# Kernel optimization log

Hardware: AMD Instinct MI355X
Metric: run time of the kernel (lower is better)

## Reference

```python
import jax, jax.numpy as jnp
import numpy as np

LMBDA = 0.95
RHO_MAX = 1.0
C_MAX = 1.0
N, T = 8192, 1024


def setup_inputs() -> dict:
    key = jax.random.key(0)
    ks = jax.random.split(key, 7)
    gammas = jax.random.uniform(ks[0], (N, T), dtype=jnp.float32) * 0.02 + 0.97  # discounts near 0.99
    vf_x = jax.random.normal(ks[1], (N, T + 1), dtype=jnp.float32)
    rewards = jax.random.normal(ks[2], (N, T), dtype=jnp.float32)
    action_lls = jax.random.normal(ks[3], (N, T), dtype=jnp.float32) * 0.1
    original_action_lls = jax.random.normal(ks[4], (N, T), dtype=jnp.float32) * 0.1
    terminated = jax.random.randint(ks[5], (N,), 0, 2) > 0
    episode_lengths = jax.random.randint(ks[6], (N,), 1, T + 1)
    return {
        "gammas": gammas,
        "vf_x": vf_x,
        "rewards": rewards,
        "action_lls": action_lls,
        "original_action_lls": original_action_lls,
        "terminated": terminated,
        "episode_lengths": episode_lengths,
    }


def reference(gammas, vf_x, rewards, action_lls, original_action_lls, terminated, episode_lengths):
    n_episodes, max_len = rewards.shape
    importance_weight = jnp.exp(action_lls - original_action_lls)
    rho = jnp.minimum(importance_weight, RHO_MAX)
    ep_idx = jnp.arange(n_episodes)
    # zero out discount at final step of terminated episodes
    gammas = gammas.at[ep_idx, episode_lengths - 1].multiply((~terminated).astype(gammas.dtype))
    c = LMBDA * jnp.minimum(importance_weight, C_MAX)
    gamma_c = gammas * c  # (N, T)
    delta_V = rho * (rewards + gammas * vf_x[:, 1:] - vf_x[:, :-1])  # (N, T)

    # backward recurrence: v_diff[t] = delta_V[t] + gamma_c[t] * v_diff[t+1], v_diff[T] = 0
    def step(carry, inp):
        dV_t, gc_t = inp  # each (N,)
        v = dV_t + gc_t * carry
        return v, v

    init = jnp.zeros((n_episodes,), dtype=vf_x.dtype)
    _, ys = jax.lax.scan(step, init, (delta_V.T[::-1], gamma_c.T[::-1]))  # ys: (T, N) reversed time
    v_diff = jnp.concatenate([ys[::-1].T, jnp.zeros((n_episodes, 1), dtype=vf_x.dtype)], axis=1)  # (N, T+1)
    v_s = v_diff + vf_x
    advantages = rho * (rewards * gammas * v_s[:, 1:] - vf_x[:, :-1])
    return advantages, v_s
```

## Files before the change

kernel.cpp:

```cpp
#include <hip/hip_runtime.h>

static constexpr int N_EP  = 8192;
static constexpr int T_LEN = 1024;
static constexpr float LMBDA = 0.95f;

__global__ __launch_bounds__(256) void vtrace_kernel(
    const float* __restrict__ gammas,
    const float* __restrict__ vf_x,
    const float* __restrict__ rewards,
    const float* __restrict__ action_lls,
    const float* __restrict__ orig_lls,
    const int*   __restrict__ terminated,
    const int*   __restrict__ ep_len,
    float* __restrict__ adv_out,
    float* __restrict__ vs_out)
{
    const int n    = blockIdx.x * 4 + (threadIdx.x >> 6);
    const int lane = threadIdx.x & 63;
    if (n >= N_EP) return;
    const int t0 = lane << 4;

    const long rowT  = (long)n * T_LEN + t0;
    const long rowT1 = (long)n * (T_LEN + 1) + t0;

    float g[16], r[16], rho[16], vf[17];

    const float4* g4 = reinterpret_cast<const float4*>(gammas     + rowT);
    const float4* r4 = reinterpret_cast<const float4*>(rewards    + rowT);
    const float4* a4 = reinterpret_cast<const float4*>(action_lls + rowT);
    const float4* o4 = reinterpret_cast<const float4*>(orig_lls   + rowT);
#pragma unroll
    for (int q = 0; q < 4; ++q) {
        const float4 gg = g4[q];
        const float4 rr = r4[q];
        const float4 aa = a4[q];
        const float4 oo = o4[q];
        g[4*q+0] = gg.x; g[4*q+1] = gg.y; g[4*q+2] = gg.z; g[4*q+3] = gg.w;
        r[4*q+0] = rr.x; r[4*q+1] = rr.y; r[4*q+2] = rr.z; r[4*q+3] = rr.w;
        rho[4*q+0] = fminf(__expf(aa.x - oo.x), 1.0f);
        rho[4*q+1] = fminf(__expf(aa.y - oo.y), 1.0f);
        rho[4*q+2] = fminf(__expf(aa.z - oo.z), 1.0f);
        rho[4*q+3] = fminf(__expf(aa.w - oo.w), 1.0f);
    }
#pragma unroll
    for (int j = 0; j < 17; ++j) vf[j] = vf_x[rowT1 + j];

    const int kill = ep_len[n] - 1 - t0;
    if (terminated[n] != 0 && kill >= 0 && kill < 16) g[kill] = 0.0f;

    float A = 1.0f, B = 0.0f;
#pragma unroll
    for (int j = 15; j >= 0; --j) {
        const float gc = LMBDA * rho[j] * g[j];
        const float dv = rho[j] * fmaf(g[j], vf[j + 1], r[j] - vf[j]);
        B = fmaf(gc, B, dv);
        A *= gc;
    }

#pragma unroll
    for (int d = 1; d < 64; d <<= 1) {
        const float An = __shfl_down(A, d, 64);
        const float Bn = __shfl_down(B, d, 64);
        if (lane + d < 64) { B = fmaf(A, Bn, B); A *= An; }
    }
    float carry = __shfl_down(B, 1, 64);
    if (lane == 63) carry = 0.0f;

    float v = carry;
    float vs_next = carry + vf[16];
    if (lane == 63) vs_out[rowT1 + 16] = vs_next;

    float vs_arr[16], adv_arr[16];
#pragma unroll
    for (int j = 15; j >= 0; --j) {
        const float gc = LMBDA * rho[j] * g[j];
        const float dv = rho[j] * fmaf(g[j], vf[j + 1], r[j] - vf[j]);
        v = fmaf(gc, v, dv);
        const float vsj = v + vf[j];
        adv_arr[j] = rho[j] * fmaf(r[j] * g[j], vs_next, -vf[j]);
        vs_arr[j]  = vsj;
        vs_next = vsj;
    }

    float4* adv4 = reinterpret_cast<float4*>(adv_out + rowT);
#pragma unroll
    for (int q = 0; q < 4; ++q)
        adv4[q] = make_float4(adv_arr[4*q+0], adv_arr[4*q+1],
                              adv_arr[4*q+2], adv_arr[4*q+3]);
#pragma unroll
    for (int j = 0; j < 16; ++j) vs_out[rowT1 + j] = vs_arr[j];
}

extern "C" void kernel_launch(void* const* d_in, const int* in_sizes, int n_in,
                              void* d_out, int out_size, void* d_ws, size_t ws_size,
                              hipStream_t stream) {
    const float* gammas     = (const float*)d_in[0];
    const float* vf_x       = (const float*)d_in[1];
    const float* rewards    = (const float*)d_in[2];
    const float* action_lls = (const float*)d_in[3];
    const float* orig_lls   = (const float*)d_in[4];
    const int*   terminated = (const int*)d_in[5];
    const int*   ep_len     = (const int*)d_in[6];

    float* adv = (float*)d_out;
    float* vs  = adv + (long)N_EP * T_LEN;

    dim3 grid(N_EP / 4), block(256);
    hipLaunchKernelGGL(vtrace_kernel, grid, block, 0, stream,
                       gammas, vf_x, rewards, action_lls, orig_lls,
                       terminated, ep_len, adv, vs);
}
```

Baseline: 49.51 us.

## Process each episode in coalesced 256-element chunks with chained wave scans

```diff
diff --git a/kernel.cpp b/kernel.cpp
--- a/kernel.cpp
+++ b/kernel.cpp
@@ -18,77 +18,82 @@
     const int n    = blockIdx.x * 4 + (threadIdx.x >> 6);
     const int lane = threadIdx.x & 63;
     if (n >= N_EP) return;
-    const int t0 = lane << 4;
 
-    const long rowT  = (long)n * T_LEN + t0;
-    const long rowT1 = (long)n * (T_LEN + 1) + t0;
+    const long rowT  = (long)n * T_LEN;
+    const long rowT1 = (long)n * (T_LEN + 1);
+    const int  term  = terminated[n];
+    const int  kill  = ep_len[n] - 1;
 
-    float g[16], r[16], rho[16], vf[17];
-
-    const float4* g4 = reinterpret_cast<const float4*>(gammas     + rowT);
-    const float4* r4 = reinterpret_cast<const float4*>(rewards    + rowT);
-    const float4* a4 = reinterpret_cast<const float4*>(action_lls + rowT);
-    const float4* o4 = reinterpret_cast<const float4*>(orig_lls   + rowT);
-#pragma unroll
-    for (int q = 0; q < 4; ++q) {
-        const float4 gg = g4[q];
-        const float4 rr = r4[q];
-        const float4 aa = a4[q];
-        const float4 oo = o4[q];
-        g[4*q+0] = gg.x; g[4*q+1] = gg.y; g[4*q+2] = gg.z; g[4*q+3] = gg.w;
-        r[4*q+0] = rr.x; r[4*q+1] = rr.y; r[4*q+2] = rr.z; r[4*q+3] = rr.w;
-        rho[4*q+0] = fminf(__expf(aa.x - oo.x), 1.0f);
-        rho[4*q+1] = fminf(__expf(aa.y - oo.y), 1.0f);
-        rho[4*q+2] = fminf(__expf(aa.z - oo.z), 1.0f);
-        rho[4*q+3] = fminf(__expf(aa.w - oo.w), 1.0f);
-    }
-#pragma unroll
-    for (int j = 0; j < 17; ++j) vf[j] = vf_x[rowT1 + j];
-
-    const int kill = ep_len[n] - 1 - t0;
-    if (terminated[n] != 0 && kill >= 0 && kill < 16) g[kill] = 0.0f;
-
-    float A = 1.0f, B = 0.0f;
-#pragma unroll
-    for (int j = 15; j >= 0; --j) {
-        const float gc = LMBDA * rho[j] * g[j];
-        const float dv = rho[j] * fmaf(g[j], vf[j + 1], r[j] - vf[j]);
-        B = fmaf(gc, B, dv);
-        A *= gc;
-    }
+    float v_in = 0.0f;
 
 #pragma unroll
-    for (int d = 1; d < 64; d <<= 1) {
-        const float An = __shfl_down(A, d, 64);
-        const float Bn = __shfl_down(B, d, 64);
-        if (lane + d < 64) { B = fmaf(A, Bn, B); A *= An; }
+    for (int q = 3; q >= 0; --q) {
+        const int base = q * 256 + lane * 4;
+
+        const float4 gg = *reinterpret_cast<const float4*>(gammas     + rowT + base);
+        const float4 rr = *reinterpret_cast<const float4*>(rewards    + rowT + base);
+        const float4 aa = *reinterpret_cast<const float4*>(action_lls + rowT + base);
+        const float4 oo = *reinterpret_cast<const float4*>(orig_lls   + rowT + base);
+        float g[4] = {gg.x, gg.y, gg.z, gg.w};
+        float r[4] = {rr.x, rr.y, rr.z, rr.w};
+        float rho[4];
+        rho[0] = fminf(__expf(aa.x - oo.x), 1.0f);
+        rho[1] = fminf(__expf(aa.y - oo.y), 1.0f);
+        rho[2] = fminf(__expf(aa.z - oo.z), 1.0f);
+        rho[3] = fminf(__expf(aa.w - oo.w), 1.0f);
+
+        float vf[5];
+#pragma unroll
+        for (int k = 0; k < 5; ++k) vf[k] = vf_x[rowT1 + base + k];
+
+        if (term) {
+#pragma unroll
+            for (int j = 0; j < 4; ++j)
+                if (kill == base + j) g[j] = 0.0f;
+        }
+
+        float A = 1.0f, B = 0.0f;
+#pragma unroll
+        for (int j = 3; j >= 0; --j) {
+            const float gc = LMBDA * rho[j] * g[j];
+            const float dv = rho[j] * fmaf(g[j], vf[j + 1], r[j] - vf[j]);
+            B = fmaf(gc, B, dv);
+            A *= gc;
+        }
+
+#pragma unroll
+        for (int d = 1; d < 64; d <<= 1) {
+            const float An = __shfl_down(A, d, 64);
+            const float Bn = __shfl_down(B, d, 64);
+            if (lane + d < 64) { B = fmaf(A, Bn, B); A *= An; }
+        }
+        const float A1 = __shfl_down(A, 1, 64);
+        const float B1 = __shfl_down(B, 1, 64);
+        const float carry = (lane == 63) ? v_in : fmaf(A1, v_in, B1);
+
+        float vs_next = carry + vf[4];
+        if (q == 3 && lane == 63)
+            vs_out[rowT1 + T_LEN] = vs_next;
+
+        float v = carry;
+        float vsa[4], adv[4];
+#pragma unroll
+        for (int j = 3; j >= 0; --j) {
+            const float gc = LMBDA * rho[j] * g[j];
+            const float dv = rho[j] * fmaf(g[j], vf[j + 1], r[j] - vf[j]);
+            v = fmaf(gc, v, dv);
+            vsa[j] = v + vf[j];
+            adv[j] = rho[j] * fmaf(r[j] * g[j], vs_next, -vf[j]);
+            vs_next = vsa[j];
+        }
+
+        *reinterpret_cast<float4*>(adv_out + rowT + base) =
+            make_float4(adv[0], adv[1], adv[2], adv[3]);
+#pragma unroll
+        for (int j = 0; j < 4; ++j) vs_out[rowT1 + base + j] = vsa[j];
+
+        v_in = __shfl(v, 0, 64);
     }
-    float carry = __shfl_down(B, 1, 64);
-    if (lane == 63) carry = 0.0f;
-
-    float v = carry;
-    float vs_next = carry + vf[16];
-    if (lane == 63) vs_out[rowT1 + 16] = vs_next;
-
-    float vs_arr[16], adv_arr[16];
-#pragma unroll
-    for (int j = 15; j >= 0; --j) {
-        const float gc = LMBDA * rho[j] * g[j];
-        const float dv = rho[j] * fmaf(g[j], vf[j + 1], r[j] - vf[j]);
-        v = fmaf(gc, v, dv);
-        const float vsj = v + vf[j];
-        adv_arr[j] = rho[j] * fmaf(r[j] * g[j], vs_next, -vf[j]);
-        vs_arr[j]  = vsj;
-        vs_next = vsj;
-    }
-
-    float4* adv4 = reinterpret_cast<float4*>(adv_out + rowT);
-#pragma unroll
-    for (int q = 0; q < 4; ++q)
-        adv4[q] = make_float4(adv_arr[4*q+0], adv_arr[4*q+1],
-                              adv_arr[4*q+2], adv_arr[4*q+3]);
-#pragma unroll
-    for (int j = 0; j < 16; ++j) vs_out[rowT1 + j] = vs_arr[j];
 }
 
 extern "C" void kernel_launch(void* const* d_in, const int* in_sizes, int n_in,
```

New measurement: 40.58 us, median of 2. 1.22x faster.
